# Performance work log

Measured on AMD Instinct MI355X. Metric: run time of the kernel, lower is better.

The kernel has to match this reference:

```python
import jax, jax.numpy as jnp
import numpy as np

B, T, D, H = 2, 2048, 1024, 16
DH = D // H
SCALE = DH ** -0.5
NEG_INF = float(np.finfo(np.float32).min)


def setup_inputs() -> dict:
    key = jax.random.key(0)
    ks = jax.random.split(key, 8)
    query = jax.random.normal(ks[0], (B, T, D), dtype=jnp.float32)
    key_t = jax.random.normal(ks[1], (B, T, D), dtype=jnp.float32)
    value = jax.random.normal(ks[2], (B, T, D), dtype=jnp.float32)
    # causal mask: True means blocked (upper triangle)
    mask = ~jnp.tril(jnp.ones((T, T), dtype=bool))
    # key padding: pad tail beyond a random valid length per batch row
    lens = jax.random.randint(ks[3], (B,), T // 2, T)
    key_padding_mask = jnp.arange(T)[None, :] >= lens[:, None]  # [B, T] True = pad
    s = D ** -0.5
    Wq = jax.random.normal(ks[4], (D, D), dtype=jnp.float32) * s
    Wk = jax.random.normal(ks[5], (D, D), dtype=jnp.float32) * s
    Wv = jax.random.normal(ks[6], (D, D), dtype=jnp.float32) * s
    Wo = jax.random.normal(ks[7], (D, D), dtype=jnp.float32) * s
    return {"query": query, "key": key_t, "value": value, "mask": mask,
            "key_padding_mask": key_padding_mask, "Wq": Wq, "Wk": Wk, "Wv": Wv, "Wo": Wo}


def reference(query, key, value, mask, key_padding_mask, Wq, Wk, Wv, Wo):
    # Linear (no bias): y = x @ W.T, then split heads -> [B, H, T, DH]
    def proj(x, W, Tlen):
        return jnp.einsum('btd,ed->bte', x, W).reshape(B, Tlen, H, DH).transpose(0, 2, 1, 3)

    q = proj(query, Wq, T)
    k = proj(key, Wk, T)
    v = proj(value, Wv, T)

    attn = jnp.einsum('bhqd,bhkd->bhqk', q, k) * SCALE  # [B, H, Tq, Tk]
    attn = jnp.where(mask[None, None, :, :], -jnp.inf, attn)
    attn = jnp.where(key_padding_mask[:, None, None, :], -jnp.inf, attn)
    # rows of batches where ALL keys are padding: zero the logits (softmax -> uniform)
    all_masked = jnp.all(key_padding_mask, axis=-1)[:, None, None, None]
    attn = jnp.where(all_masked, 0.0, attn)

    p = jax.nn.softmax(attn, axis=-1)
    p = jnp.where(jnp.isnan(p), 0.0, p)  # scrub NaN rows (all -inf)

    out = jnp.einsum('bhqk,bhkd->bhqd', p, v)
    out = out.transpose(0, 2, 1, 3).reshape(B, T, D)
    return jnp.einsum('btd,ed->bte', out, Wo)
```

## Files before the change

### kernel.cpp

```cpp
#include <hip/hip_runtime.h>

#define B_  2
#define T_  2048
#define D_  1024
#define H_  16
#define DH_ 64
#define M_  4096

typedef _Float16 f16;
typedef _Float16 f16x8 __attribute__((ext_vector_type(8)));
typedef _Float16 f16x4 __attribute__((ext_vector_type(4)));
typedef __fp16   fp16x2 __attribute__((ext_vector_type(2)));
typedef float    f32x4  __attribute__((ext_vector_type(4)));
typedef float    f32x16 __attribute__((ext_vector_type(16)));
typedef unsigned int u32;

__device__ __forceinline__ void async_ld16(const void* g, void* l) {
  __builtin_amdgcn_global_load_lds(
      (const __attribute__((address_space(1))) unsigned int*)g,
      (__attribute__((address_space(3))) unsigned int*)l,
      16, 0, 0);
}

__device__ __forceinline__ u32 pkrtz(float a, float b) {
  union { fp16x2 h; u32 u; } x;
  x.h = __builtin_amdgcn_cvt_pkrtz(a, b);
  return x.u;
}

__global__ __launch_bounds__(256) void convert_all(
    const float* __restrict__ q, const float* __restrict__ k, const float* __restrict__ v,
    const float* __restrict__ wq, const float* __restrict__ wk, const float* __restrict__ wv,
    const float* __restrict__ wo, const void* __restrict__ kpm_raw,
    f16* __restrict__ xh, f16* __restrict__ wh, int* __restrict__ lens_out) {
  int bid = blockIdx.x;
  if (bid >= 8192) {
    int b = bid - 8192;
    __shared__ int s_c8, s_c32;
    if (threadIdx.x == 0) { s_c8 = 0; s_c32 = 0; }
    __syncthreads();
    int tid = threadIdx.x, lane = tid & 63;
    {
      const unsigned char* k8 = (const unsigned char*)kpm_raw + (long)b * T_;
      int cnt = 0;
      for (int j = tid; j < T_; j += 256) cnt += (k8[j] == 0) ? 1 : 0;
#pragma unroll
      for (int off = 1; off < 64; off <<= 1) cnt += __shfl_xor(cnt, off);
      if (lane == 0) atomicAdd(&s_c8, cnt);
    }
    {
      const int* k32 = (const int*)kpm_raw + (long)b * T_;
      int cnt = 0;
      for (int j = tid; j < T_; j += 256) cnt += (k32[j] == 0) ? 1 : 0;
#pragma unroll
      for (int off = 1; off < 64; off <<= 1) cnt += __shfl_xor(cnt, off);
      if (lane == 0) atomicAdd(&s_c32, cnt);
    }
    __syncthreads();
    if (tid == 0) lens_out[b] = (s_c8 == T_) ? s_c32 : s_c8;
    return;
  }
  const float* src;
  f16* dst;
  long base;
  if (bid < 6144) {
    int r = bid >> 11;
    src = (r == 0) ? q : (r == 1) ? k : v;
    dst = xh + (long)r * 4194304;
    base = (long)(bid & 2047) * 2048;
  } else {
    int r = (bid - 6144) >> 9;
    src = (r == 0) ? wq : (r == 1) ? wk : (r == 2) ? wv : wo;
    dst = wh + (long)r * 1048576;
    base = (long)((bid - 6144) & 511) * 2048;
  }
  long e = base + (long)threadIdx.x * 8;
  const float4* s4 = (const float4*)(src + e);
  float4 f0 = s4[0], f1 = s4[1];
  f16x8 o;
  o[0] = (f16)f0.x; o[1] = (f16)f0.y; o[2] = (f16)f0.z; o[3] = (f16)f0.w;
  o[4] = (f16)f1.x; o[5] = (f16)f1.y; o[6] = (f16)f1.z; o[7] = (f16)f1.w;
  *(f16x8*)(dst + e) = o;
}

__global__ __launch_bounds__(512) void gemm_k(
    const f16* __restrict__ Abase, const f16* __restrict__ Wbase,
    f16* __restrict__ Qb, f16* __restrict__ Kb, f16* __restrict__ Vt,
    float* __restrict__ Co, int which) {
  __shared__ __align__(16) f16 As[2][4096];
  __shared__ __align__(16) f16 Bs[2][4096];
  const int K = 1024, N = 1024;

  int gx = gridDim.x, gy = gridDim.y;
  int nwg = gx * gy * gridDim.z;
  int bid = blockIdx.x + gx * (blockIdx.y + gy * blockIdx.z);
  int cpx = nwg >> 3;
  int wg = (bid & 7) * cpx + (bid >> 3);
  int bz = wg / (gx * gy);
  int rem = wg - bz * gx * gy;
  int by = rem / gx, bx = rem - by * gx;

  int mode;
  const f16 *A, *W;
  if (which) { mode = 3; A = Abase; W = Wbase; }
  else {
    mode = bz;
    A = Abase + (long)bz * 4194304;
    W = Wbase + (long)bz * 1048576;
  }
  int m0 = by * 128, n0 = bx * 128;
  int tid = threadIdx.x, lane = tid & 63, w = tid >> 6;
  int wr = w >> 2, wc = w & 3;

  int srow = tid >> 2;
  int sp   = tid & 3;
  int ss   = ((srow & 3) + ((srow >> 2) & 3)) & 3;
  int scol = (sp ^ ss) * 8;
  const f16* pa = A + (long)(m0 + srow) * K + scol;
  const f16* pb = W + (long)(n0 + srow) * K + scol;
  int ldst = tid * 8;

  f32x4 acc[4][2] = {};
  int row = lane & 15;
  int rs  = ((row & 3) + ((row >> 2) & 3)) & 3;
  int kq  = ((lane >> 4) ^ rs) * 8;

  auto STAGE = [&](int k0, int bsel) {
    async_ld16(pa + k0, &As[bsel][ldst]);
    async_ld16(pb + k0, &Bs[bsel][ldst]);
  };

  STAGE(0, 0);
  asm volatile("s_waitcnt vmcnt(0)" ::: "memory");
  __builtin_amdgcn_s_barrier();

  int cur = 0;
  for (int k0 = 0; k0 < K; k0 += 32) {
    if (k0 + 32 < K) STAGE(k0 + 32, cur ^ 1);
    f16x8 af[4], bfr[2];
#pragma unroll
    for (int m = 0; m < 4; m++)
      af[m] = *(const f16x8*)&As[cur][(wr * 64 + m * 16 + row) * 32 + kq];
#pragma unroll
    for (int n = 0; n < 2; n++)
      bfr[n] = *(const f16x8*)&Bs[cur][(wc * 32 + n * 16 + row) * 32 + kq];
#pragma unroll
    for (int m = 0; m < 4; m++)
#pragma unroll
      for (int n = 0; n < 2; n++)
        acc[m][n] = __builtin_amdgcn_mfma_f32_16x16x32_f16(af[m], bfr[n], acc[m][n], 0, 0, 0);
    asm volatile("s_waitcnt vmcnt(0)" ::: "memory");
    __builtin_amdgcn_s_barrier();
    cur ^= 1;
  }

  int r0 = (lane >> 4) * 4;
#pragma unroll
  for (int m = 0; m < 4; m++) {
    int gmb = m0 + wr * 64 + m * 16 + r0;
#pragma unroll
    for (int n = 0; n < 2; n++) {
      int gn = n0 + wc * 32 + n * 16 + row;
      if (mode == 0) {
#pragma unroll
        for (int i = 0; i < 4; i++)
          Qb[(long)(gmb + i) * N + gn] = (f16)(acc[m][n][i] * 0.18033688f);
      } else if (mode == 1) {
#pragma unroll
        for (int i = 0; i < 4; i++)
          Kb[(long)(gmb + i) * N + gn] = (f16)acc[m][n][i];
      } else if (mode == 2) {
        int b = gmb >> 11;
        int t = gmb & 2047;
        int h = gn >> 6, dh = gn & 63;
        f16x4 pk;
#pragma unroll
        for (int i = 0; i < 4; i++) pk[i] = (f16)acc[m][n][i];
        *(f16x4*)&Vt[(long)((b * 16 + h) * 64 + dh) * 2048 + t] = pk;
      } else {
#pragma unroll
        for (int i = 0; i < 4; i++)
          Co[(long)(gmb + i) * N + gn] = acc[m][n][i];
      }
    }
  }
}

__global__ __launch_bounds__(256, 2) void attn_k(
    const f16* __restrict__ Q, const f16* __restrict__ Kp,
    const f16* __restrict__ Vt, const int* __restrict__ Lens,
    f16* __restrict__ Ao) {
  __shared__ __align__(16) f16 Kl[4][4096];
  __shared__ __align__(16) f16 Vl[4][4096];

  int tid = threadIdx.x, lane = tid & 63, w = tid >> 6;
  int bh = blockIdx.x;
  int j  = blockIdx.y;
  int qm = (j < 8) ? (15 - j) : (j - 8);
  int b = bh >> 4, h = bh & 15;
  int r31 = lane & 31, hi = lane >> 5, hi8 = hi * 8;

  int len = Lens[b];
  int q0 = qm * 128;
  int q0w = q0 + w * 32;
  int gq = q0w + r31;

  int blk_kmax = min(q0 + 128, len);
  int wav_kmax = min(q0w + 32, len);
  int NR = (blk_kmax + 127) >> 7;

  const f16* Qh = Q  + (long)b * T_ * D_ + h * 64;
  const f16* Kh = Kp + (long)b * T_ * D_ + h * 64;
  const f16* Vh = Vt + (long)(b * 16 + h) * 64 * T_;

  int srow = w * 16 + (lane >> 3);
  int sc8  = ((lane & 7) ^ ((lane >> 3) & 7)) * 8;
  int ldst = w * 1024 + lane * 8;

  int coff[4];
#pragma unroll
  for (int t = 0; t < 4; t++) coff[t] = ((2 * t + hi) ^ (r31 & 7)) * 8;

  auto STAGE64 = [&](int t, int bsel) {
    int kb = t * 64;
#pragma unroll
    for (int s = 0; s < 2; s++) {
      int row = srow + s * 8;
      async_ld16(Kh + (long)(kb + row) * D_ + sc8, &Kl[bsel][ldst + s * 512]);
      async_ld16(Vh + (long)row * T_ + kb + sc8,   &Vl[bsel][ldst + s * 512]);
    }
  };

  STAGE64(0, 0);
  STAGE64(1, 1);
  f16x8 qf[4];
#pragma unroll
  for (int t = 0; t < 4; t++)
    qf[t] = *(const f16x8*)(Qh + (long)gq * D_ + t * 16 + hi8);

  f32x16 o0 = {}, o1 = {};
  float mrun = -1e30f, lrun = 0.f;

  auto QK = [&](int buf, f32x16& sa, f32x16& sb) {
#pragma unroll
    for (int tq = 0; tq < 4; tq++) {
      f16x8 k0 = *(const f16x8*)&Kl[buf][(r31)      * 64 + coff[tq]];
      f16x8 k1 = *(const f16x8*)&Kl[buf][(32 + r31) * 64 + coff[tq]];
      sa = __builtin_amdgcn_mfma_f32_32x32x16_f16(k0, qf[tq], sa, 0, 0, 0);
      sb = __builtin_amdgcn_mfma_f32_32x32x16_f16(k1, qf[tq], sb, 0, 0, 0);
    }
  };

  auto MASK = [&](f32x16& sa, f32x16& sb, int kb) {
#pragma unroll
    for (int r = 0; r < 16; r++) {
      int pat = (r & 3) + 8 * (r >> 2) + 4 * hi;
      int gk0 = kb + pat, gk1 = kb + 32 + pat;
      if (gk0 > gq || gk0 >= len) sa[r] = -1e30f;
      if (gk1 > gq || gk1 >= len) sb[r] = -1e30f;
    }
  };

  auto PV = [&](int bufV, f32x16& sa, f32x16& sb) {
    u32 a0 = pkrtz(sa[0],  sa[1]),  a1 = pkrtz(sa[2],  sa[3]);
    u32 b0 = pkrtz(sa[4],  sa[5]),  b1 = pkrtz(sa[6],  sa[7]);
    u32 c0 = pkrtz(sa[8],  sa[9]),  c1 = pkrtz(sa[10], sa[11]);
    u32 d0 = pkrtz(sa[12], sa[13]), d1 = pkrtz(sa[14], sa[15]);
    u32 e0 = pkrtz(sb[0],  sb[1]),  e1 = pkrtz(sb[2],  sb[3]);
    u32 f0_ = pkrtz(sb[4],  sb[5]), f1_ = pkrtz(sb[6],  sb[7]);
    u32 g0 = pkrtz(sb[8],  sb[9]),  g1 = pkrtz(sb[10], sb[11]);
    u32 h0 = pkrtz(sb[12], sb[13]), h1 = pkrtz(sb[14], sb[15]);
    asm("v_permlane32_swap_b32 %0, %1" : "+v"(a0), "+v"(b0));
    asm("v_permlane32_swap_b32 %0, %1" : "+v"(a1), "+v"(b1));
    asm("v_permlane32_swap_b32 %0, %1" : "+v"(c0), "+v"(d0));
    asm("v_permlane32_swap_b32 %0, %1" : "+v"(c1), "+v"(d1));
    asm("v_permlane32_swap_b32 %0, %1" : "+v"(e0), "+v"(f0_));
    asm("v_permlane32_swap_b32 %0, %1" : "+v"(e1), "+v"(f1_));
    asm("v_permlane32_swap_b32 %0, %1" : "+v"(g0), "+v"(h0));
    asm("v_permlane32_swap_b32 %0, %1" : "+v"(g1), "+v"(h1));
    union { u32 w[4]; f16x8 v; } f00, f01, f10, f11;
    f00.w[0] = a0;  f00.w[1] = a1;  f00.w[2] = b0;  f00.w[3] = b1;
    f01.w[0] = c0;  f01.w[1] = c1;  f01.w[2] = d0;  f01.w[3] = d1;
    f10.w[0] = e0;  f10.w[1] = e1;  f10.w[2] = f0_; f10.w[3] = f1_;
    f11.w[0] = g0;  f11.w[1] = g1;  f11.w[2] = h0;  f11.w[3] = h1;

    f16x8 v00 = *(const f16x8*)&Vl[bufV][(r31)      * 64 + coff[0]];
    f16x8 v01 = *(const f16x8*)&Vl[bufV][(r31)      * 64 + coff[1]];
    f16x8 v02 = *(const f16x8*)&Vl[bufV][(r31)      * 64 + coff[2]];
    f16x8 v03 = *(const f16x8*)&Vl[bufV][(r31)      * 64 + coff[3]];
    f16x8 v10 = *(const f16x8*)&Vl[bufV][(32 + r31) * 64 + coff[0]];
    f16x8 v11 = *(const f16x8*)&Vl[bufV][(32 + r31) * 64 + coff[1]];
    f16x8 v12 = *(const f16x8*)&Vl[bufV][(32 + r31) * 64 + coff[2]];
    f16x8 v13 = *(const f16x8*)&Vl[bufV][(32 + r31) * 64 + coff[3]];

    o0 = __builtin_amdgcn_mfma_f32_32x32x16_f16(v00, f00.v, o0, 0, 0, 0);
    o0 = __builtin_amdgcn_mfma_f32_32x32x16_f16(v01, f01.v, o0, 0, 0, 0);
    o0 = __builtin_amdgcn_mfma_f32_32x32x16_f16(v02, f10.v, o0, 0, 0, 0);
    o0 = __builtin_amdgcn_mfma_f32_32x32x16_f16(v03, f11.v, o0, 0, 0, 0);
    o1 = __builtin_amdgcn_mfma_f32_32x32x16_f16(v10, f00.v, o1, 0, 0, 0);
    o1 = __builtin_amdgcn_mfma_f32_32x32x16_f16(v11, f01.v, o1, 0, 0, 0);
    o1 = __builtin_amdgcn_mfma_f32_32x32x16_f16(v12, f10.v, o1, 0, 0, 0);
    o1 = __builtin_amdgcn_mfma_f32_32x32x16_f16(v13, f11.v, o1, 0, 0, 0);
  };

  asm volatile("s_waitcnt vmcnt(0)" ::: "memory");
  __syncthreads();

  for (int r = 0; r < NR; r++) {
    int t0 = 2 * r;
    int b0buf = t0 & 3, b1buf = (t0 + 1) & 3;
    if (r + 1 < NR) { STAGE64(t0 + 2, (t0 + 2) & 3); STAGE64(t0 + 3, (t0 + 3) & 3); }

    int kb = r * 128;
    if (kb < wav_kmax) {
      bool has2 = (kb + 64) < wav_kmax;
      f32x16 s0 = {}, s1 = {}, s2, s3;
#pragma unroll
      for (int i = 0; i < 16; i++) { s2[i] = -1e30f; s3[i] = -1e30f; }

      QK(b0buf, s0, s1);
      if (has2) {
        f32x16 z0 = {}, z1 = {};
        QK(b1buf, z0, z1);
        s2 = z0; s3 = z1;
      }
      if (kb + 128 > q0w || kb + 128 > len) {
        MASK(s0, s1, kb);
        if (has2) MASK(s2, s3, kb + 64);
      }

      float t16[16];
#pragma unroll
      for (int rr = 0; rr < 16; rr++)
        t16[rr] = fmaxf(fmaxf(s0[rr], s1[rr]), fmaxf(s2[rr], s3[rr]));
#pragma unroll
      for (int s = 8; s > 0; s >>= 1)
#pragma unroll
        for (int rr = 0; rr < s; rr++) t16[rr] = fmaxf(t16[rr], t16[rr + s]);
      float mx = fmaxf(t16[0], __shfl_xor(t16[0], 32));

      float mnew = fmaxf(mrun, mx);
      float sf = exp2f(mrun - mnew);
      mrun = mnew;

      float ps[4] = {0.f, 0.f, 0.f, 0.f};
#pragma unroll
      for (int rr = 0; rr < 16; rr++) {
        s0[rr] = exp2f(s0[rr] - mnew);  ps[rr & 3] += s0[rr];
        s1[rr] = exp2f(s1[rr] - mnew);  ps[rr & 3] += s1[rr];
      }
      if (has2) {
#pragma unroll
        for (int rr = 0; rr < 16; rr++) {
          s2[rr] = exp2f(s2[rr] - mnew);  ps[rr & 3] += s2[rr];
          s3[rr] = exp2f(s3[rr] - mnew);  ps[rr & 3] += s3[rr];
        }
      }
      float psum = (ps[0] + ps[1]) + (ps[2] + ps[3]);
      lrun = lrun * sf + psum + __shfl_xor(psum, 32);

      o0 *= sf;
      o1 *= sf;

      PV(b0buf, s0, s1);
      if (has2) PV(b1buf, s2, s3);
    }

    asm volatile("s_waitcnt vmcnt(0)" ::: "memory");
    __syncthreads();
  }

  float linv = 1.f / lrun;
  f16* Aob = Ao + (long)(b * T_ + gq) * D_ + h * 64 + 4 * hi;
#pragma unroll
  for (int g = 0; g < 4; g++) {
    f16x4 s0, s1;
#pragma unroll
    for (int i = 0; i < 4; i++) {
      s0[i] = (f16)(o0[g * 4 + i] * linv);
      s1[i] = (f16)(o1[g * 4 + i] * linv);
    }
    *(f16x4*)(Aob + 8 * g)      = s0;
    *(f16x4*)(Aob + 32 + 8 * g) = s1;
  }
}

extern "C" void kernel_launch(void* const* d_in, const int* in_sizes, int n_in,
                              void* d_out, int out_size, void* d_ws, size_t ws_size,
                              hipStream_t stream) {
  const float* q  = (const float*)d_in[0];
  const float* k  = (const float*)d_in[1];
  const float* v  = (const float*)d_in[2];
  const void* kpm = d_in[4];
  const float* wq = (const float*)d_in[5];
  const float* wk = (const float*)d_in[6];
  const float* wv = (const float*)d_in[7];
  const float* wo = (const float*)d_in[8];

  char* ws = (char*)d_ws;
  f16* Xh = (f16*)(ws);
  f16* Wh = (f16*)(ws + 25165824);
  f16* Qb = (f16*)(ws + 33554432);
  f16* Kb = (f16*)(ws + 41943040);
  f16* Vt = (f16*)(ws + 50331648);
  f16* Ao = (f16*)(ws + 58720256);
  int* Lens = (int*)d_out;

  convert_all<<<8194, 256, 0, stream>>>(q, k, v, wq, wk, wv, wo, kpm, Xh, Wh, Lens);

  gemm_k<<<dim3(8, 32, 3), 512, 0, stream>>>(Xh, Wh, Qb, Kb, Vt, nullptr, 0);

  attn_k<<<dim3(B_ * H_, T_ / 128), 256, 0, stream>>>(Qb, Kb, Vt, Lens, Ao);

  gemm_k<<<dim3(8, 32, 1), 512, 0, stream>>>(Ao, Wh + 3 * 1048576, nullptr, nullptr,
                                             nullptr, (float*)d_out, 1);
}
```

Baseline: 119.2 us.

## Fuse fp32-to-fp16 activation conversion into the QKV projection GEMM

The separate pass that converted the query/key/value activations to fp16 is removed. The QKV GEMM now loads fp32 A tiles into registers, converts them in-loop and writes them to LDS, while weights still go through async global-to-LDS loads. This drops a 48MB read+write round trip through the workspace, at the cost of the QKV GEMM reading twice as many A bytes per tile and doing register-staged LDS writes instead of direct async loads. The GEMM becomes a template with an fp16 path kept for the output projection.

```diff
diff --git a/kernel.cpp b/kernel.cpp
--- a/kernel.cpp
+++ b/kernel.cpp
@@ -28,14 +28,13 @@
   return x.u;
 }
 
-__global__ __launch_bounds__(256) void convert_all(
-    const float* __restrict__ q, const float* __restrict__ k, const float* __restrict__ v,
+__global__ __launch_bounds__(256) void convert_w(
     const float* __restrict__ wq, const float* __restrict__ wk, const float* __restrict__ wv,
     const float* __restrict__ wo, const void* __restrict__ kpm_raw,
-    f16* __restrict__ xh, f16* __restrict__ wh, int* __restrict__ lens_out) {
+    f16* __restrict__ wh, int* __restrict__ lens_out) {
   int bid = blockIdx.x;
-  if (bid >= 8192) {
-    int b = bid - 8192;
+  if (bid >= 2048) {
+    int b = bid - 2048;
     __shared__ int s_c8, s_c32;
     if (threadIdx.x == 0) { s_c8 = 0; s_c32 = 0; }
     __syncthreads();
@@ -60,20 +59,10 @@
     if (tid == 0) lens_out[b] = (s_c8 == T_) ? s_c32 : s_c8;
     return;
   }
-  const float* src;
-  f16* dst;
-  long base;
-  if (bid < 6144) {
-    int r = bid >> 11;
-    src = (r == 0) ? q : (r == 1) ? k : v;
-    dst = xh + (long)r * 4194304;
-    base = (long)(bid & 2047) * 2048;
-  } else {
-    int r = (bid - 6144) >> 9;
-    src = (r == 0) ? wq : (r == 1) ? wk : (r == 2) ? wv : wo;
-    dst = wh + (long)r * 1048576;
-    base = (long)((bid - 6144) & 511) * 2048;
-  }
+  int r = bid >> 9;
+  const float* src = (r == 0) ? wq : (r == 1) ? wk : (r == 2) ? wv : wo;
+  f16* dst = wh + (long)r * 1048576;
+  long base = (long)(bid & 511) * 2048;
   long e = base + (long)threadIdx.x * 8;
   const float4* s4 = (const float4*)(src + e);
   float4 f0 = s4[0], f1 = s4[1];
@@ -83,10 +72,13 @@
   *(f16x8*)(dst + e) = o;
 }
 
+template <bool AF32>
 __global__ __launch_bounds__(512) void gemm_k(
-    const f16* __restrict__ Abase, const f16* __restrict__ Wbase,
+    const float* __restrict__ Aq, const float* __restrict__ Ak,
+    const float* __restrict__ Av, const f16* __restrict__ A16,
+    const f16* __restrict__ Wbase,
     f16* __restrict__ Qb, f16* __restrict__ Kb, f16* __restrict__ Vt,
-    float* __restrict__ Co, int which) {
+    float* __restrict__ Co) {
   __shared__ __align__(16) f16 As[2][4096];
   __shared__ __align__(16) f16 Bs[2][4096];
   const int K = 1024, N = 1024;
@@ -100,14 +92,13 @@
   int rem = wg - bz * gx * gy;
   int by = rem / gx, bx = rem - by * gx;
 
-  int mode;
-  const f16 *A, *W;
-  if (which) { mode = 3; A = Abase; W = Wbase; }
-  else {
-    mode = bz;
-    A = Abase + (long)bz * 4194304;
-    W = Wbase + (long)bz * 1048576;
-  }
+  int mode = AF32 ? bz : 3;
+  const float* A32 = nullptr;
+  const f16*   Af  = nullptr;
+  if (AF32) A32 = (bz == 0) ? Aq : (bz == 1) ? Ak : Av;
+  else      Af  = A16;
+  const f16* W = AF32 ? (Wbase + (long)bz * 1048576) : Wbase;
+
   int m0 = by * 128, n0 = bx * 128;
   int tid = threadIdx.x, lane = tid & 63, w = tid >> 6;
   int wr = w >> 2, wc = w & 3;
@@ -116,8 +107,9 @@
   int sp   = tid & 3;
   int ss   = ((srow & 3) + ((srow >> 2) & 3)) & 3;
   int scol = (sp ^ ss) * 8;
-  const f16* pa = A + (long)(m0 + srow) * K + scol;
-  const f16* pb = W + (long)(n0 + srow) * K + scol;
+  const float* pa32 = AF32 ? (A32 + (long)(m0 + srow) * K + scol) : nullptr;
+  const f16*   pa16 = AF32 ? nullptr : (Af + (long)(m0 + srow) * K + scol);
+  const f16*   pb   = W + (long)(n0 + srow) * K + scol;
   int ldst = tid * 8;
 
   f32x4 acc[4][2] = {};
@@ -125,18 +117,41 @@
   int rs  = ((row & 3) + ((row >> 2) & 3)) & 3;
   int kq  = ((lane >> 4) ^ rs) * 8;
 
-  auto STAGE = [&](int k0, int bsel) {
-    async_ld16(pa + k0, &As[bsel][ldst]);
-    async_ld16(pb + k0, &Bs[bsel][ldst]);
-  };
-
-  STAGE(0, 0);
-  asm volatile("s_waitcnt vmcnt(0)" ::: "memory");
+  float4 fa0, fa1;
+  auto LOADA32 = [&](int k0) {
+    const float4* p = (const float4*)(pa32 + k0);
+    fa0 = p[0]; fa1 = p[1];
+  };
+  auto WRITEA = [&](int bsel) {
+    f16x8 h;
+    h[0] = (f16)fa0.x; h[1] = (f16)fa0.y; h[2] = (f16)fa0.z; h[3] = (f16)fa0.w;
+    h[4] = (f16)fa1.x; h[5] = (f16)fa1.y; h[6] = (f16)fa1.z; h[7] = (f16)fa1.w;
+    *(f16x8*)&As[bsel][ldst] = h;
+  };
+
+  if (AF32) {
+    LOADA32(0);
+    WRITEA(0);
+    async_ld16(pb, &Bs[0][ldst]);
+  } else {
+    async_ld16(pa16, &As[0][ldst]);
+    async_ld16(pb,   &Bs[0][ldst]);
+  }
+  asm volatile("s_waitcnt vmcnt(0) lgkmcnt(0)" ::: "memory");
   __builtin_amdgcn_s_barrier();
 
   int cur = 0;
   for (int k0 = 0; k0 < K; k0 += 32) {
-    if (k0 + 32 < K) STAGE(k0 + 32, cur ^ 1);
+    bool more = (k0 + 32 < K);
+    if (more) {
+      if (AF32) {
+        LOADA32(k0 + 32);
+        async_ld16(pb + k0 + 32, &Bs[cur ^ 1][ldst]);
+      } else {
+        async_ld16(pa16 + k0 + 32, &As[cur ^ 1][ldst]);
+        async_ld16(pb   + k0 + 32, &Bs[cur ^ 1][ldst]);
+      }
+    }
     f16x8 af[4], bfr[2];
 #pragma unroll
     for (int m = 0; m < 4; m++)
@@ -149,7 +164,8 @@
 #pragma unroll
       for (int n = 0; n < 2; n++)
         acc[m][n] = __builtin_amdgcn_mfma_f32_16x16x32_f16(af[m], bfr[n], acc[m][n], 0, 0, 0);
-    asm volatile("s_waitcnt vmcnt(0)" ::: "memory");
+    if (AF32 && more) WRITEA(cur ^ 1);
+    asm volatile("s_waitcnt vmcnt(0) lgkmcnt(0)" ::: "memory");
     __builtin_amdgcn_s_barrier();
     cur ^= 1;
   }
@@ -398,20 +414,21 @@
   const float* wo = (const float*)d_in[8];
 
   char* ws = (char*)d_ws;
-  f16* Xh = (f16*)(ws);
-  f16* Wh = (f16*)(ws + 25165824);
-  f16* Qb = (f16*)(ws + 33554432);
-  f16* Kb = (f16*)(ws + 41943040);
-  f16* Vt = (f16*)(ws + 50331648);
-  f16* Ao = (f16*)(ws + 58720256);
+  f16* Wh = (f16*)(ws);
+  f16* Qb = (f16*)(ws + 8388608);
+  f16* Kb = (f16*)(ws + 16777216);
+  f16* Vt = (f16*)(ws + 25165824);
+  f16* Ao = (f16*)(ws + 33554432);
   int* Lens = (int*)d_out;
 
-  convert_all<<<8194, 256, 0, stream>>>(q, k, v, wq, wk, wv, wo, kpm, Xh, Wh, Lens);
-
-  gemm_k<<<dim3(8, 32, 3), 512, 0, stream>>>(Xh, Wh, Qb, Kb, Vt, nullptr, 0);
+  convert_w<<<2050, 256, 0, stream>>>(wq, wk, wv, wo, kpm, Wh, Lens);
+
+  gemm_k<true><<<dim3(8, 32, 3), 512, 0, stream>>>(
+      q, k, v, nullptr, Wh, Qb, Kb, Vt, nullptr);
 
   attn_k<<<dim3(B_ * H_, T_ / 128), 256, 0, stream>>>(Qb, Kb, Vt, Lens, Ao);
 
-  gemm_k<<<dim3(8, 32, 1), 512, 0, stream>>>(Ao, Wh + 3 * 1048576, nullptr, nullptr,
-                                             nullptr, (float*)d_out, 1);
-}
+  gemm_k<false><<<dim3(8, 32, 1), 512, 0, stream>>>(
+      nullptr, nullptr, nullptr, Ao, Wh + 3 * 1048576, nullptr, nullptr, nullptr,
+      (float*)d_out);
+}
```

Result: faster. 115.3 us (-3.3%).
